# Kernel tuning notes

Measured on AMD Instinct MI355X. Metric: run time of the kernel, lower is better.

The kernel has to match this reference:

```python
import jax, jax.numpy as jnp
import numpy as np

B, T = 128, 2048
O, E, L = 128, 512, 34  # o_size, embed_dim, num_letter


def setup_inputs() -> dict:
    key = jax.random.key(0)
    ks = jax.random.split(key, 16)
    u = lambda k, shape, s: jax.random.uniform(k, shape, jnp.float32, -s, s)
    hk = jax.random.normal(ks[0], (B, T, O), jnp.float32)
    hv = jax.random.normal(ks[1], (B, T, O), jnp.float32)
    y_1 = jax.random.normal(ks[2], (B, E), jnp.float32)
    c_1 = jax.random.normal(ks[3], (B, O), jnp.float32)
    sh_1 = jax.random.normal(ks[4], (B, O), jnp.float32)
    sc_1 = jax.random.normal(ks[5], (B, O), jnp.float32)
    # valid-length mask (each row has at least T//2 valid positions)
    lengths = jax.random.randint(ks[6], (B,), T // 2, T + 1)
    mask = (jnp.arange(T)[None, :] < lengths[:, None]).astype(jnp.float32)
    s_rnn = 1.0 / np.sqrt(O)
    W_ih = u(ks[7], (4 * O, O + E), s_rnn)
    b_ih = u(ks[8], (4 * O,), s_rnn)
    W_hh = u(ks[9], (4 * O, O), s_rnn)
    b_hh = u(ks[10], (4 * O,), s_rnn)
    s1 = 1.0 / np.sqrt(O)
    W1 = u(ks[11], (L, O), s1); b1 = u(ks[12], (L,), s1)
    W2 = u(ks[13], (L, O), s1); b2 = u(ks[14], (L,), s1)
    s3 = 1.0 / np.sqrt(L)
    W3 = u(ks[15], (L, L), s3); b3 = u(jax.random.fold_in(key, 99), (L,), s3)
    return {"hk": hk, "hv": hv, "y_1": y_1, "c_1": c_1, "sh_1": sh_1,
            "sc_1": sc_1, "mask": mask, "W_ih": W_ih, "b_ih": b_ih,
            "W_hh": W_hh, "b_hh": b_hh, "W1": W1, "b1": b1,
            "W2": W2, "b2": b2, "W3": W3, "b3": b3}


def reference(hk, hv, y_1, c_1, sh_1, sc_1, mask,
              W_ih, b_ih, W_hh, b_hh, W1, b1, W2, b2, W3, b3):
    # LSTMCell (PyTorch gate order: i, f, g, o)
    x = jnp.concatenate([y_1, c_1], axis=1)            # [B, O+E]
    gates = x @ W_ih.T + b_ih + sh_1 @ W_hh.T + b_hh   # [B, 4O]
    i, f, g, o = jnp.split(gates, 4, axis=1)
    sc = jax.nn.sigmoid(f) * sc_1 + jax.nn.sigmoid(i) * jnp.tanh(g)
    sh = jax.nn.sigmoid(o) * jnp.tanh(sc)
    # attention scores keyed on cell state sc (faithful to source)
    scores = jnp.einsum('bto,bo->bt', hk, sc)          # [B, T]
    attn = jax.nn.softmax(scores, axis=1) * mask
    attn = attn / jnp.sum(attn, axis=1, keepdims=True)
    c = jnp.einsum('bt,bto->bo', attn, hv)             # [B, O]
    out = jax.nn.relu(sh @ W1.T + b1 + c @ W2.T + b2)
    out = jax.nn.softmax(out @ W3.T + b3, axis=1)      # [B, L]
    return (out, c, sh, sc)
```

## Files before the change

kernel.cpp:

```cpp
#include <hip/hip_runtime.h>
#include <math.h>

#define BB 128
#define TT 2048
#define OO 128
#define EE 512
#define LL 34
#define XDIM 640
#define CHUNKS 16
#define CHUNK_LEN 128
#define PSTRIDE 132
#define GWS_FLOATS (BB * 4 * OO)

__device__ __forceinline__ float sigmoidf_(float x) { return 1.0f / (1.0f + __expf(-x)); }

__device__ __forceinline__ float hred32(float x) {
    x += __shfl_xor(x, 16);
    x += __shfl_xor(x, 8);
    x += __shfl_xor(x, 4);
    x += __shfl_xor(x, 2);
    x += __shfl_xor(x, 1);
    return x;
}

__global__ __launch_bounds__(256) void lstm_gemm_kernel(
    const float* __restrict__ y1, const float* __restrict__ c1,
    const float* __restrict__ sh1,
    const float* __restrict__ Wih, const float* __restrict__ bih,
    const float* __restrict__ Whh, const float* __restrict__ bhh,
    float* __restrict__ gws)
{
    __shared__ float xs[4][768];
    const int tid = threadIdx.x;
    const int t = blockIdx.x;
    const int qb = blockIdx.y * 4;

    for (int idx = tid; idx < 4 * 768; idx += 256) {
        int bi = idx / 768, k = idx - bi * 768;
        int b = qb + bi;
        float v;
        if (k < 512)      v = y1[b * EE + k];
        else if (k < 640) v = c1[b * OO + (k - 512)];
        else              v = sh1[b * OO + (k - 640)];
        xs[bi][k] = v;
    }
    __syncthreads();

    const int w = tid >> 6, l = tid & 63;
    for (int i = 0; i < 32; ++i) {
        const int row = t * 128 + w * 32 + i;
        const float* wr = Wih + (size_t)row * XDIM;
        float a0 = 0.f, a1 = 0.f, a2 = 0.f, a3 = 0.f;
        #pragma unroll
        for (int j = 0; j < 10; ++j) {
            float wv = wr[l + 64 * j];
            a0 += wv * xs[0][l + 64 * j];
            a1 += wv * xs[1][l + 64 * j];
            a2 += wv * xs[2][l + 64 * j];
            a3 += wv * xs[3][l + 64 * j];
        }
        const float* wh = Whh + (size_t)row * OO;
        #pragma unroll
        for (int j = 0; j < 2; ++j) {
            float wv = wh[l + 64 * j];
            a0 += wv * xs[0][640 + l + 64 * j];
            a1 += wv * xs[1][640 + l + 64 * j];
            a2 += wv * xs[2][640 + l + 64 * j];
            a3 += wv * xs[3][640 + l + 64 * j];
        }
        #pragma unroll
        for (int off = 32; off >= 1; off >>= 1) {
            a0 += __shfl_xor(a0, off);
            a1 += __shfl_xor(a1, off);
            a2 += __shfl_xor(a2, off);
            a3 += __shfl_xor(a3, off);
        }
        if (l == 0) {
            float bb = bih[row] + bhh[row];
            gws[(size_t)(qb + 0) * 512 + row] = a0 + bb;
            gws[(size_t)(qb + 1) * 512 + row] = a1 + bb;
            gws[(size_t)(qb + 2) * 512 + row] = a2 + bb;
            gws[(size_t)(qb + 3) * 512 + row] = a3 + bb;
        }
    }
}

__global__ __launch_bounds__(128) void lstm_act_kernel(
    const float* __restrict__ gws, const float* __restrict__ sc1,
    float* __restrict__ out_sh, float* __restrict__ out_sc)
{
    const int b = blockIdx.x, o = threadIdx.x;
    const float* g = gws + (size_t)b * 512;
    float gi = g[o], gf = g[o + 128], gg = g[o + 256], go = g[o + 384];
    float sc = sigmoidf_(gf) * sc1[b * OO + o] + sigmoidf_(gi) * tanhf(gg);
    float sh = sigmoidf_(go) * tanhf(sc);
    out_sc[b * OO + o] = sc;
    out_sh[b * OO + o] = sh;
}

__global__ __launch_bounds__(256) void attn_kernel(
    const float* __restrict__ hk, const float* __restrict__ hv,
    const float* __restrict__ mask, const float* __restrict__ sc,
    float* __restrict__ ws_part)
{
    const int b = blockIdx.y;
    const int chunk = blockIdx.x;
    const int tid = threadIdx.x;
    const int g = tid >> 5, l = tid & 31;

    const float4 scv = *(const float4*)(sc + b * OO + l * 4);
    float m = -INFINITY, S = 0.f;
    float4 acc = make_float4(0.f, 0.f, 0.f, 0.f);

    const float* kbase = hk + (size_t)(b * TT + chunk * CHUNK_LEN) * OO;
    const float* vbase = hv + (size_t)(b * TT + chunk * CHUNK_LEN) * OO;
    const float* mbase = mask + (size_t)b * TT + chunk * CHUNK_LEN;

    #pragma unroll 1
    for (int q = 0; q < 4; ++q) {
        const int r = g * 16 + q * 4;
        const float4 mk = *(const float4*)(mbase + r);
        if (mk.x == 0.f) break;
        const float4 k0 = *(const float4*)(kbase + (size_t)(r + 0) * OO + l * 4);
        const float4 k1 = *(const float4*)(kbase + (size_t)(r + 1) * OO + l * 4);
        const float4 k2 = *(const float4*)(kbase + (size_t)(r + 2) * OO + l * 4);
        const float4 k3 = *(const float4*)(kbase + (size_t)(r + 3) * OO + l * 4);
        const float4 v0 = *(const float4*)(vbase + (size_t)(r + 0) * OO + l * 4);
        const float4 v1 = *(const float4*)(vbase + (size_t)(r + 1) * OO + l * 4);
        const float4 v2 = *(const float4*)(vbase + (size_t)(r + 2) * OO + l * 4);
        const float4 v3 = *(const float4*)(vbase + (size_t)(r + 3) * OO + l * 4);
        float s0 = k0.x * scv.x + k0.y * scv.y + k0.z * scv.z + k0.w * scv.w;
        float s1 = k1.x * scv.x + k1.y * scv.y + k1.z * scv.z + k1.w * scv.w;
        float s2 = k2.x * scv.x + k2.y * scv.y + k2.z * scv.z + k2.w * scv.w;
        float s3 = k3.x * scv.x + k3.y * scv.y + k3.z * scv.z + k3.w * scv.w;
        s0 = hred32(s0); s1 = hred32(s1); s2 = hred32(s2); s3 = hred32(s3);

        float mnew, scale, p;
        mnew = fmaxf(m, s0); scale = __expf(m - mnew); p = __expf(s0 - mnew) * mk.x;
        S = S * scale + p;
        acc.x = acc.x * scale + p * v0.x; acc.y = acc.y * scale + p * v0.y;
        acc.z = acc.z * scale + p * v0.z; acc.w = acc.w * scale + p * v0.w;
        m = mnew;
        mnew = fmaxf(m, s1); scale = __expf(m - mnew); p = __expf(s1 - mnew) * mk.y;
        S = S * scale + p;
        acc.x = acc.x * scale + p * v1.x; acc.y = acc.y * scale + p * v1.y;
        acc.z = acc.z * scale + p * v1.z; acc.w = acc.w * scale + p * v1.w;
        m = mnew;
        mnew = fmaxf(m, s2); scale = __expf(m - mnew); p = __expf(s2 - mnew) * mk.z;
        S = S * scale + p;
        acc.x = acc.x * scale + p * v2.x; acc.y = acc.y * scale + p * v2.y;
        acc.z = acc.z * scale + p * v2.z; acc.w = acc.w * scale + p * v2.w;
        m = mnew;
        mnew = fmaxf(m, s3); scale = __expf(m - mnew); p = __expf(s3 - mnew) * mk.w;
        S = S * scale + p;
        acc.x = acc.x * scale + p * v3.x; acc.y = acc.y * scale + p * v3.y;
        acc.z = acc.z * scale + p * v3.z; acc.w = acc.w * scale + p * v3.w;
        m = mnew;
    }

    __shared__ float sm[8], sS[8], sacc[8][128];
    if (l == 0) { sm[g] = m; sS[g] = S; }
    sacc[g][l * 4 + 0] = acc.x;
    sacc[g][l * 4 + 1] = acc.y;
    sacc[g][l * 4 + 2] = acc.z;
    sacc[g][l * 4 + 3] = acc.w;
    __syncthreads();

    float M = sm[0];
    #pragma unroll
    for (int i = 1; i < 8; i++) M = fmaxf(M, sm[i]);
    const float Mc = (M == -INFINITY) ? 0.f : M;

    float* wout = ws_part + (size_t)(b * CHUNKS + chunk) * PSTRIDE;
    if (tid < 128) {
        float ca = 0.f;
        #pragma unroll
        for (int i = 0; i < 8; i++) ca += sacc[i][tid] * __expf(sm[i] - Mc);
        wout[tid] = ca;
    } else if (tid == 128) {
        float St = 0.f;
        #pragma unroll
        for (int i = 0; i < 8; i++) St += sS[i] * __expf(sm[i] - Mc);
        wout[128] = St;
        wout[129] = M;
    }
}

__global__ __launch_bounds__(256) void final_kernel(
    const float* __restrict__ ws_part, const float* __restrict__ sh_in,
    const float* __restrict__ W1, const float* __restrict__ b1,
    const float* __restrict__ W2, const float* __restrict__ b2,
    const float* __restrict__ W3, const float* __restrict__ b3,
    float* __restrict__ out_p, float* __restrict__ out_c)
{
    const int b = blockIdx.x, tid = threadIdx.x;
    __shared__ float sM[CHUNKS], sS[CHUNKS], cbuf[128], shbuf[128], h1[LL], zz[LL], red2[2];
    const float* base = ws_part + (size_t)b * CHUNKS * PSTRIDE;

    if (tid < CHUNKS) {
        sS[tid] = base[tid * PSTRIDE + 128];
        sM[tid] = base[tid * PSTRIDE + 129];
    }
    __syncthreads();
    float M = sM[0];
    #pragma unroll
    for (int i = 1; i < CHUNKS; i++) M = fmaxf(M, sM[i]);

    if (tid < 128) {
        float ca = 0.f, S = 0.f;
        #pragma unroll
        for (int i = 0; i < CHUNKS; i++) {
            float e = __expf(sM[i] - M);
            ca += base[i * PSTRIDE + tid] * e;
            S += sS[i] * e;
        }
        float cv = ca / S;
        cbuf[tid] = cv;
        out_c[b * OO + tid] = cv;
        shbuf[tid] = sh_in[b * OO + tid];
    }
    __syncthreads();

    const int o = tid >> 2, l2 = tid & 3;
    if (o < LL) {
        float a = 0.f;
        const float* w1r = W1 + o * OO;
        const float* w2r = W2 + o * OO;
        #pragma unroll 8
        for (int j = 0; j < 32; ++j) {
            int k = l2 + 4 * j;
            a += w1r[k] * shbuf[k] + w2r[k] * cbuf[k];
        }
        a += __shfl_xor(a, 1);
        a += __shfl_xor(a, 2);
        if (l2 == 0) h1[o] = fmaxf(a + b1[o] + b2[o], 0.f);
    }
    __syncthreads();

    if (o < LL) {
        float z = 0.f;
        const float* w3r = W3 + o * LL;
        for (int j = 0; j < 9; ++j) {
            int k = l2 + 4 * j;
            if (k < LL) z += w3r[k] * h1[k];
        }
        z += __shfl_xor(z, 1);
        z += __shfl_xor(z, 2);
        if (l2 == 0) zz[o] = z + b3[o];
    }
    __syncthreads();
    if (tid == 0) {
        float mm = zz[0];
        for (int i = 1; i < LL; i++) mm = fmaxf(mm, zz[i]);
        float ss = 0.f;
        for (int i = 0; i < LL; i++) ss += __expf(zz[i] - mm);
        red2[0] = mm; red2[1] = ss;
    }
    __syncthreads();
    if (tid < LL) out_p[b * LL + tid] = __expf(zz[tid] - red2[0]) / red2[1];
}

extern "C" void kernel_launch(void* const* d_in, const int* in_sizes, int n_in,
                              void* d_out, int out_size, void* d_ws, size_t ws_size,
                              hipStream_t stream) {
    (void)in_sizes; (void)n_in; (void)out_size; (void)ws_size;
    const float* hk   = (const float*)d_in[0];
    const float* hv   = (const float*)d_in[1];
    const float* y1   = (const float*)d_in[2];
    const float* c1   = (const float*)d_in[3];
    const float* sh1  = (const float*)d_in[4];
    const float* sc1  = (const float*)d_in[5];
    const float* mask = (const float*)d_in[6];
    const float* Wih  = (const float*)d_in[7];
    const float* bih  = (const float*)d_in[8];
    const float* Whh  = (const float*)d_in[9];
    const float* bhh  = (const float*)d_in[10];
    const float* W1   = (const float*)d_in[11];
    const float* b1   = (const float*)d_in[12];
    const float* W2   = (const float*)d_in[13];
    const float* b2   = (const float*)d_in[14];
    const float* W3   = (const float*)d_in[15];
    const float* b3   = (const float*)d_in[16];

    float* out    = (float*)d_out;
    float* out_c  = out + BB * LL;
    float* out_sh = out_c + BB * OO;
    float* out_sc = out_sh + BB * OO;

    float* gws     = (float*)d_ws;
    float* ws_part = gws + GWS_FLOATS;

    lstm_gemm_kernel<<<dim3(4, 32), 256, 0, stream>>>(y1, c1, sh1, Wih, bih, Whh, bhh, gws);
    lstm_act_kernel<<<BB, 128, 0, stream>>>(gws, sc1, out_sh, out_sc);
    attn_kernel<<<dim3(CHUNKS, BB), 256, 0, stream>>>(hk, hv, mask, out_sc, ws_part);
    final_kernel<<<BB, 256, 0, stream>>>(ws_part, out_sh, W1, b1, W2, b2, W3, b3,
                                         out, out_c);
}
```

Baseline: 336.6 us.

## Split attention into scores, softmax, weighted-sum kernels; fuse LSTM activation into GEMM

Folds the gate activation into the LSTM GEMM kernel by reorganizing blocks so each block computes all four gates for a 16-wide output tile, which removes one launch and a global round trip. Replaces the single online-softmax attention kernel with three kernels: a scores kernel reading hk, a full-row softmax kernel, and a weighted-sum kernel reading hv that skips zero-weight rows. This drops the per-element rescaling exps and the partial-max bookkeeping, at the cost of an extra launch and a scores buffer written and read through global memory.

```diff
diff --git a/kernel.cpp b/kernel.cpp
--- a/kernel.cpp
+++ b/kernel.cpp
@@ -9,30 +9,20 @@
 #define XDIM 640
 #define CHUNKS 16
 #define CHUNK_LEN 128
-#define PSTRIDE 132
-#define GWS_FLOATS (BB * 4 * OO)
 
 __device__ __forceinline__ float sigmoidf_(float x) { return 1.0f / (1.0f + __expf(-x)); }
 
-__device__ __forceinline__ float hred32(float x) {
-    x += __shfl_xor(x, 16);
-    x += __shfl_xor(x, 8);
-    x += __shfl_xor(x, 4);
-    x += __shfl_xor(x, 2);
-    x += __shfl_xor(x, 1);
-    return x;
-}
-
-__global__ __launch_bounds__(256) void lstm_gemm_kernel(
+__global__ __launch_bounds__(256) void lstm_kernel(
     const float* __restrict__ y1, const float* __restrict__ c1,
-    const float* __restrict__ sh1,
+    const float* __restrict__ sh1, const float* __restrict__ sc1,
     const float* __restrict__ Wih, const float* __restrict__ bih,
     const float* __restrict__ Whh, const float* __restrict__ bhh,
-    float* __restrict__ gws)
+    float* __restrict__ out_sh, float* __restrict__ out_sc)
 {
     __shared__ float xs[4][768];
+    __shared__ float gbuf[4][4][16];
     const int tid = threadIdx.x;
-    const int t = blockIdx.x;
+    const int otile = blockIdx.x;
     const int qb = blockIdx.y * 4;
 
     for (int idx = tid; idx < 4 * 768; idx += 256) {
@@ -46,9 +36,10 @@
     }
     __syncthreads();
 
-    const int w = tid >> 6, l = tid & 63;
-    for (int i = 0; i < 32; ++i) {
-        const int row = t * 128 + w * 32 + i;
+    const int g = tid >> 6, l = tid & 63;
+    #pragma unroll 2
+    for (int i = 0; i < 16; ++i) {
+        const int row = g * 128 + otile * 16 + i;
         const float* wr = Wih + (size_t)row * XDIM;
         float a0 = 0.f, a1 = 0.f, a2 = 0.f, a3 = 0.f;
         #pragma unroll
@@ -77,146 +68,164 @@
         }
         if (l == 0) {
             float bb = bih[row] + bhh[row];
-            gws[(size_t)(qb + 0) * 512 + row] = a0 + bb;
-            gws[(size_t)(qb + 1) * 512 + row] = a1 + bb;
-            gws[(size_t)(qb + 2) * 512 + row] = a2 + bb;
-            gws[(size_t)(qb + 3) * 512 + row] = a3 + bb;
-        }
-    }
-}
-
-__global__ __launch_bounds__(128) void lstm_act_kernel(
-    const float* __restrict__ gws, const float* __restrict__ sc1,
-    float* __restrict__ out_sh, float* __restrict__ out_sc)
-{
-    const int b = blockIdx.x, o = threadIdx.x;
-    const float* g = gws + (size_t)b * 512;
-    float gi = g[o], gf = g[o + 128], gg = g[o + 256], go = g[o + 384];
-    float sc = sigmoidf_(gf) * sc1[b * OO + o] + sigmoidf_(gi) * tanhf(gg);
-    float sh = sigmoidf_(go) * tanhf(sc);
-    out_sc[b * OO + o] = sc;
-    out_sh[b * OO + o] = sh;
-}
-
-__global__ __launch_bounds__(256) void attn_kernel(
-    const float* __restrict__ hk, const float* __restrict__ hv,
-    const float* __restrict__ mask, const float* __restrict__ sc,
-    float* __restrict__ ws_part)
-{
-    const int b = blockIdx.y;
-    const int chunk = blockIdx.x;
+            gbuf[g][0][i] = a0 + bb;
+            gbuf[g][1][i] = a1 + bb;
+            gbuf[g][2][i] = a2 + bb;
+            gbuf[g][3][i] = a3 + bb;
+        }
+    }
+    __syncthreads();
+
+    if (tid < 64) {
+        const int bi = tid >> 4, ol = tid & 15;
+        const int b = qb + bi, o = otile * 16 + ol;
+        float gi = gbuf[0][bi][ol], gf = gbuf[1][bi][ol];
+        float gg = gbuf[2][bi][ol], go = gbuf[3][bi][ol];
+        float sc = sigmoidf_(gf) * sc1[b * OO + o] + sigmoidf_(gi) * tanhf(gg);
+        float sh = sigmoidf_(go) * tanhf(sc);
+        out_sc[b * OO + o] = sc;
+        out_sh[b * OO + o] = sh;
+    }
+}
+
+__global__ __launch_bounds__(256) void scores_kernel(
+    const float* __restrict__ hk, const float* __restrict__ mask,
+    const float* __restrict__ sc, float* __restrict__ wbuf)
+{
+    const int b = blockIdx.y, chunk = blockIdx.x;
     const int tid = threadIdx.x;
-    const int g = tid >> 5, l = tid & 31;
-
-    const float4 scv = *(const float4*)(sc + b * OO + l * 4);
-    float m = -INFINITY, S = 0.f;
+    const int sg = tid >> 4, l = tid & 15;
+
+    const float4 scA = *(const float4*)(sc + b * OO + l * 8);
+    const float4 scB = *(const float4*)(sc + b * OO + l * 8 + 4);
+
+    const int r0 = chunk * CHUNK_LEN + sg * 8;
+    const float* mrow = mask + (size_t)b * TT + r0;
+    const float* krow = hk + ((size_t)b * TT + r0) * OO;
+
+    float s[8];
+    #pragma unroll
+    for (int i = 0; i < 8; ++i) {
+        const bool valid = (mrow[i] != 0.f);
+        float4 a = make_float4(0.f, 0.f, 0.f, 0.f);
+        float4 c2 = make_float4(0.f, 0.f, 0.f, 0.f);
+        if (valid) {
+            a  = *(const float4*)(krow + (size_t)i * OO + l * 8);
+            c2 = *(const float4*)(krow + (size_t)i * OO + l * 8 + 4);
+        }
+        s[i] = a.x * scA.x + a.y * scA.y + a.z * scA.z + a.w * scA.w
+             + c2.x * scB.x + c2.y * scB.y + c2.z * scB.z + c2.w * scB.w;
+    }
+    #pragma unroll
+    for (int i = 0; i < 8; ++i) {
+        s[i] += __shfl_xor(s[i], 8);
+        s[i] += __shfl_xor(s[i], 4);
+        s[i] += __shfl_xor(s[i], 2);
+        s[i] += __shfl_xor(s[i], 1);
+    }
+    float* wrow = wbuf + (size_t)b * TT + r0;
+    #pragma unroll
+    for (int i = 0; i < 8; ++i)
+        if (l == i) wrow[i] = s[i];
+}
+
+__global__ __launch_bounds__(256) void softmax_kernel(
+    float* __restrict__ wbuf, const float* __restrict__ mask)
+{
+    const int b = blockIdx.x, tid = threadIdx.x;
+    const int lane = tid & 63, wv = tid >> 6;
+    float* srow = wbuf + (size_t)b * TT;
+    const float* mrow = mask + (size_t)b * TT;
+
+    float sarr[8], earr[8];
+    bool varr[8];
+    float lm = -INFINITY;
+    #pragma unroll
+    for (int j = 0; j < 8; ++j) {
+        int t = tid + 256 * j;
+        sarr[j] = srow[t];
+        varr[j] = (mrow[t] != 0.f);
+        if (varr[j]) lm = fmaxf(lm, sarr[j]);
+    }
+    #pragma unroll
+    for (int off = 32; off >= 1; off >>= 1) lm = fmaxf(lm, __shfl_xor(lm, off));
+    __shared__ float red[4];
+    if (lane == 0) red[wv] = lm;
+    __syncthreads();
+    const float M = fmaxf(fmaxf(red[0], red[1]), fmaxf(red[2], red[3]));
+
+    float ls = 0.f;
+    #pragma unroll
+    for (int j = 0; j < 8; ++j) {
+        earr[j] = varr[j] ? __expf(sarr[j] - M) : 0.f;
+        ls += earr[j];
+    }
+    #pragma unroll
+    for (int off = 32; off >= 1; off >>= 1) ls += __shfl_xor(ls, off);
+    __syncthreads();
+    if (lane == 0) red[wv] = ls;
+    __syncthreads();
+    const float inv = 1.f / (red[0] + red[1] + red[2] + red[3]);
+    #pragma unroll
+    for (int j = 0; j < 8; ++j) srow[tid + 256 * j] = earr[j] * inv;
+}
+
+__global__ __launch_bounds__(256) void wsum_kernel(
+    const float* __restrict__ hv, const float* __restrict__ wbuf,
+    float* __restrict__ ws_c)
+{
+    const int b = blockIdx.y, chunk = blockIdx.x;
+    const int tid = threadIdx.x;
+    __shared__ float wsh[CHUNK_LEN];
+    __shared__ float pacc[8][128];
+
+    if (tid < CHUNK_LEN)
+        wsh[tid] = wbuf[(size_t)b * TT + chunk * CHUNK_LEN + tid];
+    __syncthreads();
+
+    const int o4 = tid & 31, rr = tid >> 5;
+    const float* vbase = hv + ((size_t)b * TT + chunk * CHUNK_LEN) * OO + o4 * 4;
     float4 acc = make_float4(0.f, 0.f, 0.f, 0.f);
-
-    const float* kbase = hk + (size_t)(b * TT + chunk * CHUNK_LEN) * OO;
-    const float* vbase = hv + (size_t)(b * TT + chunk * CHUNK_LEN) * OO;
-    const float* mbase = mask + (size_t)b * TT + chunk * CHUNK_LEN;
-
-    #pragma unroll 1
-    for (int q = 0; q < 4; ++q) {
-        const int r = g * 16 + q * 4;
-        const float4 mk = *(const float4*)(mbase + r);
-        if (mk.x == 0.f) break;
-        const float4 k0 = *(const float4*)(kbase + (size_t)(r + 0) * OO + l * 4);
-        const float4 k1 = *(const float4*)(kbase + (size_t)(r + 1) * OO + l * 4);
-        const float4 k2 = *(const float4*)(kbase + (size_t)(r + 2) * OO + l * 4);
-        const float4 k3 = *(const float4*)(kbase + (size_t)(r + 3) * OO + l * 4);
-        const float4 v0 = *(const float4*)(vbase + (size_t)(r + 0) * OO + l * 4);
-        const float4 v1 = *(const float4*)(vbase + (size_t)(r + 1) * OO + l * 4);
-        const float4 v2 = *(const float4*)(vbase + (size_t)(r + 2) * OO + l * 4);
-        const float4 v3 = *(const float4*)(vbase + (size_t)(r + 3) * OO + l * 4);
-        float s0 = k0.x * scv.x + k0.y * scv.y + k0.z * scv.z + k0.w * scv.w;
-        float s1 = k1.x * scv.x + k1.y * scv.y + k1.z * scv.z + k1.w * scv.w;
-        float s2 = k2.x * scv.x + k2.y * scv.y + k2.z * scv.z + k2.w * scv.w;
-        float s3 = k3.x * scv.x + k3.y * scv.y + k3.z * scv.z + k3.w * scv.w;
-        s0 = hred32(s0); s1 = hred32(s1); s2 = hred32(s2); s3 = hred32(s3);
-
-        float mnew, scale, p;
-        mnew = fmaxf(m, s0); scale = __expf(m - mnew); p = __expf(s0 - mnew) * mk.x;
-        S = S * scale + p;
-        acc.x = acc.x * scale + p * v0.x; acc.y = acc.y * scale + p * v0.y;
-        acc.z = acc.z * scale + p * v0.z; acc.w = acc.w * scale + p * v0.w;
-        m = mnew;
-        mnew = fmaxf(m, s1); scale = __expf(m - mnew); p = __expf(s1 - mnew) * mk.y;
-        S = S * scale + p;
-        acc.x = acc.x * scale + p * v1.x; acc.y = acc.y * scale + p * v1.y;
-        acc.z = acc.z * scale + p * v1.z; acc.w = acc.w * scale + p * v1.w;
-        m = mnew;
-        mnew = fmaxf(m, s2); scale = __expf(m - mnew); p = __expf(s2 - mnew) * mk.z;
-        S = S * scale + p;
-        acc.x = acc.x * scale + p * v2.x; acc.y = acc.y * scale + p * v2.y;
-        acc.z = acc.z * scale + p * v2.z; acc.w = acc.w * scale + p * v2.w;
-        m = mnew;
-        mnew = fmaxf(m, s3); scale = __expf(m - mnew); p = __expf(s3 - mnew) * mk.w;
-        S = S * scale + p;
-        acc.x = acc.x * scale + p * v3.x; acc.y = acc.y * scale + p * v3.y;
-        acc.z = acc.z * scale + p * v3.z; acc.w = acc.w * scale + p * v3.w;
-        m = mnew;
-    }
-
-    __shared__ float sm[8], sS[8], sacc[8][128];
-    if (l == 0) { sm[g] = m; sS[g] = S; }
-    sacc[g][l * 4 + 0] = acc.x;
-    sacc[g][l * 4 + 1] = acc.y;
-    sacc[g][l * 4 + 2] = acc.z;
-    sacc[g][l * 4 + 3] = acc.w;
-    __syncthreads();
-
-    float M = sm[0];
-    #pragma unroll
-    for (int i = 1; i < 8; i++) M = fmaxf(M, sm[i]);
-    const float Mc = (M == -INFINITY) ? 0.f : M;
-
-    float* wout = ws_part + (size_t)(b * CHUNKS + chunk) * PSTRIDE;
+    #pragma unroll 8
+    for (int j = 0; j < 16; ++j) {
+        const int r = rr + 8 * j;
+        const float wr = wsh[r];
+        if (wr != 0.f) {
+            float4 v = *(const float4*)(vbase + (size_t)r * OO);
+            acc.x += wr * v.x;
+            acc.y += wr * v.y;
+            acc.z += wr * v.z;
+            acc.w += wr * v.w;
+        }
+    }
+    *(float4*)&pacc[rr][o4 * 4] = acc;
+    __syncthreads();
+
     if (tid < 128) {
-        float ca = 0.f;
-        #pragma unroll
-        for (int i = 0; i < 8; i++) ca += sacc[i][tid] * __expf(sm[i] - Mc);
-        wout[tid] = ca;
-    } else if (tid == 128) {
-        float St = 0.f;
-        #pragma unroll
-        for (int i = 0; i < 8; i++) St += sS[i] * __expf(sm[i] - Mc);
-        wout[128] = St;
-        wout[129] = M;
+        float s = 0.f;
+        #pragma unroll
+        for (int i = 0; i < 8; ++i) s += pacc[i][tid];
+        ws_c[((size_t)b * CHUNKS + chunk) * OO + tid] = s;
     }
 }
 
 __global__ __launch_bounds__(256) void final_kernel(
-    const float* __restrict__ ws_part, const float* __restrict__ sh_in,
+    const float* __restrict__ ws_c, const float* __restrict__ sh_in,
     const float* __restrict__ W1, const float* __restrict__ b1,
     const float* __restrict__ W2, const float* __restrict__ b2,
     const float* __restrict__ W3, const float* __restrict__ b3,
     float* __restrict__ out_p, float* __restrict__ out_c)
 {
     const int b = blockIdx.x, tid = threadIdx.x;
-    __shared__ float sM[CHUNKS], sS[CHUNKS], cbuf[128], shbuf[128], h1[LL], zz[LL], red2[2];
-    const float* base = ws_part + (size_t)b * CHUNKS * PSTRIDE;
-
-    if (tid < CHUNKS) {
-        sS[tid] = base[tid * PSTRIDE + 128];
-        sM[tid] = base[tid * PSTRIDE + 129];
-    }
-    __syncthreads();
-    float M = sM[0];
-    #pragma unroll
-    for (int i = 1; i < CHUNKS; i++) M = fmaxf(M, sM[i]);
+    __shared__ float cbuf[128], shbuf[128], h1[LL], zz[LL], red2[2];
 
     if (tid < 128) {
-        float ca = 0.f, S = 0.f;
-        #pragma unroll
-        for (int i = 0; i < CHUNKS; i++) {
-            float e = __expf(sM[i] - M);
-            ca += base[i * PSTRIDE + tid] * e;
-            S += sS[i] * e;
-        }
-        float cv = ca / S;
-        cbuf[tid] = cv;
-        out_c[b * OO + tid] = cv;
+        float s = 0.f;
+        const float* base = ws_c + (size_t)b * CHUNKS * OO + tid;
+        #pragma unroll
+        for (int i = 0; i < CHUNKS; ++i) s += base[i * OO];
+        cbuf[tid] = s;
+        out_c[b * OO + tid] = s;
         shbuf[tid] = sh_in[b * OO + tid];
     }
     __syncthreads();
@@ -287,12 +296,14 @@
     float* out_sh = out_c + BB * OO;
     float* out_sc = out_sh + BB * OO;
 
-    float* gws     = (float*)d_ws;
-    float* ws_part = gws + GWS_FLOATS;
-
-    lstm_gemm_kernel<<<dim3(4, 32), 256, 0, stream>>>(y1, c1, sh1, Wih, bih, Whh, bhh, gws);
-    lstm_act_kernel<<<BB, 128, 0, stream>>>(gws, sc1, out_sh, out_sc);
-    attn_kernel<<<dim3(CHUNKS, BB), 256, 0, stream>>>(hk, hv, mask, out_sc, ws_part);
-    final_kernel<<<BB, 256, 0, stream>>>(ws_part, out_sh, W1, b1, W2, b2, W3, b3,
+    float* wbuf = (float*)d_ws;
+    float* ws_c = wbuf + (size_t)BB * TT;
+
+    lstm_kernel<<<dim3(8, 32), 256, 0, stream>>>(y1, c1, sh1, sc1, Wih, bih, Whh, bhh,
+                                                 out_sh, out_sc);
+    scores_kernel<<<dim3(CHUNKS, BB), 256, 0, stream>>>(hk, mask, out_sc, wbuf);
+    softmax_kernel<<<BB, 256, 0, stream>>>(wbuf, mask);
+    wsum_kernel<<<dim3(CHUNKS, BB), 256, 0, stream>>>(hv, wbuf, ws_c);
+    final_kernel<<<BB, 256, 0, stream>>>(ws_c, out_sh, W1, b1, W2, b2, W3, b3,
                                          out, out_c);
 }
```

New measurement: 331.2 us. About the same (-1.6%).
